# Optimization experiments

Hardware: AMD Instinct MI355X
Metric: run time of the kernel (lower is better)

Reference implementation:

```python
import jax, jax.numpy as jnp
import numpy as np
from jax import lax

EPS = 1e-08


def setup_inputs() -> dict:
    key = jax.random.key(0)
    k1, k2, k3, k4 = jax.random.split(key, 4)
    b, cin, cout, hw, kk = 32, 256, 256, 64, 3
    fan_in = cin * kk * kk
    # kaiming_normal_(a=0, mode='fan_in', nonlinearity='leaky_relu') -> gain=sqrt(2), std=sqrt(2/fan_in)
    w_std = np.sqrt(2.0 / fan_in).astype(np.float32)
    return {
        "x": jax.random.normal(k1, (b, cin, hw, hw), dtype=jnp.float32),
        "y": jax.random.normal(k2, (b, cin), dtype=jnp.float32),
        "weight": jax.random.normal(k3, (cout, cin, kk, kk), dtype=jnp.float32) * w_std,
        "bias": jax.random.normal(k4, (cout,), dtype=jnp.float32) * 0.1,
    }


def _modulated_conv(x, y, weight, bias):
    # x: [b, cin, h, w]; y: [b, cin]; weight: [cout, cin, kh, kw]; bias: [cout]
    # modulate: per-sample scale of input channels
    w = weight[None] * (y[:, None, :, None, None] + 1.0)  # [b, cout, cin, kh, kw]
    # demodulate: normalize each (sample, out-channel) filter
    d = lax.rsqrt(jnp.sum(w * w, axis=(2, 3, 4), keepdims=True) + EPS)
    w = w * d

    def conv_one(xi, wi):
        # xi: [cin, h, w]; wi: [cout, cin, kh, kw]
        out = lax.conv_general_dilated(
            xi[None], wi, window_strides=(1, 1), padding="SAME",
            dimension_numbers=("NCHW", "OIHW", "NCHW"))
        return out[0]  # [cout, h, w]

    out = jax.vmap(conv_one)(x, w)  # [b, cout, h, w]
    return out + bias[None, :, None, None]


def reference(x, y, weight, bias):
    return _modulated_conv(x, y, weight, bias)
```

## Files before the change

kernel.cpp:

```cpp
#include <hip/hip_runtime.h>
#include <hip/hip_bf16.h>

typedef __attribute__((ext_vector_type(8))) short short8;
typedef __attribute__((ext_vector_type(4))) float f32x4;

#define XT_IMG_BYTES (66*66*256*2)
#define XT_TOTAL_BYTES (32LL*XT_IMG_BYTES)
#define WM_ROW_BYTES (2304*2)
#define WM_IMG_BYTES (256*WM_ROW_BYTES)

static __device__ __forceinline__ void async16(void* lds, const void* g) {
  __builtin_amdgcn_global_load_lds((const __attribute__((address_space(1))) void*)g,
                                   (__attribute__((address_space(3))) void*)lds, 16, 0, 0);
}
static __device__ __forceinline__ ushort f2bf(float f) {
  __hip_bfloat16 h = __float2bfloat16(f);
  return *reinterpret_cast<ushort*>(&h);
}

__global__ __launch_bounds__(256) void k_prep(const float* __restrict__ x,
                                              const float* __restrict__ W,
                                              const float* __restrict__ y,
                                              ushort* __restrict__ xT,
                                              ushort* __restrict__ wmod) {
  __shared__ float smem[64][65];
  const int bid = blockIdx.x;
  const int t   = threadIdx.x;

  if (bid < 8192) {
    const int b  = bid >> 8;
    const int h  = (bid >> 2) & 63;
    const int c0 = (bid & 3) << 6;
    const int tw = t & 63, tg = t >> 6;
    const float* xp = x + (size_t)(b * 256 + c0) * 4096 + h * 64 + tw;
#pragma unroll
    for (int j = 0; j < 16; ++j) {
      int il = j * 4 + tg;
      smem[il][tw] = xp[(size_t)il * 4096];
    }
    __syncthreads();
    const int q  = t & 7;
    const int w0 = t >> 3;
    ushort* op = xT + (size_t)b * (66 * 66 * 256) + ((size_t)(h + 1) * 66 + 1) * 256 + c0;
#pragma unroll
    for (int j = 0; j < 2; ++j) {
      const int wl = j * 32 + w0;
      short8 v;
#pragma unroll
      for (int k2 = 0; k2 < 8; ++k2) v[k2] = (short)f2bf(smem[8 * q + k2][wl]);
      *(short8*)(op + (size_t)wl * 256 + 8 * q) = v;
    }
  } else if (bid < 16384) {
    float* red = &smem[0][0];
    const int bb = bid - 8192;
    const int b = bb >> 8, o = bb & 255;
    const float* wp = W + (size_t)(o * 256 + t) * 9;
    float wr[9];
#pragma unroll
    for (int r = 0; r < 9; ++r) wr[r] = wp[r];
    const float ym = y[b * 256 + t] + 1.0f;
    float ss = 0.f;
#pragma unroll
    for (int r = 0; r < 9; ++r) ss += wr[r] * wr[r];
    red[t] = ss * ym * ym;
    __syncthreads();
    for (int s = 128; s > 0; s >>= 1) {
      if (t < s) red[t] += red[t + s];
      __syncthreads();
    }
    const float sc = rsqrtf(red[0] + 1e-8f) * ym;
    ushort* op = wmod + (size_t)(b * 256 + o) * 2304 + t;
#pragma unroll
    for (int r = 0; r < 9; ++r) op[r * 256] = f2bf(wr[r] * sc);
  } else {
    const int zb = bid - 16384;
    const int b  = zb >> 3;
    const int tt = ((zb & 7) << 8) | t;
    uint4* xT4 = (uint4*)xT;
    const uint4 z = make_uint4(0u, 0u, 0u, 0u);
    uint4* base = xT4 + (size_t)b * (66 * 66 * 32);
    uint4* r0  = base;
    uint4* r65 = base + (size_t)65 * 66 * 32;
    for (int i = tt; i < 2112; i += 2048) { r0[i] = z; r65[i] = z; }
    {
      int r = (tt >> 5) + 1, c = tt & 31;
      base[((size_t)r * 66 + 0)  * 32 + c] = z;
      base[((size_t)r * 66 + 65) * 32 + c] = z;
    }
  }
}

__global__ __launch_bounds__(512, 2) void k_gemm(const ushort* __restrict__ wmod,
                                                 const ushort* __restrict__ xT,
                                                 const float* __restrict__ bias,
                                                 float* __restrict__ out) {
  __shared__ ushort ldsA[2][16384];
  __shared__ ushort ldsB[2][16384];

  const int t  = threadIdx.x;
  const int bx = blockIdx.x;
  const int xcd = bx & 7;
  const int idx = bx >> 3;
  const int b   = xcd + ((idx >> 4) << 3);
  const int tn  = idx & 15;
  const int n0  = tn << 8;
  const int h0  = tn << 2;

  const int ln = t & 15;
  const int kq = (t >> 4) & 3;
  const int wv = t >> 6;
  const int wm = wv >> 2;
  const int wn = wv & 3;

  const char* wmodB = (const char*)wmod + (size_t)b * WM_IMG_BYTES;
  const char* xTB   = (const char*)xT   + (size_t)b * XT_IMG_BYTES;

  int gAoff[4], gBoff[4];
#pragma unroll
  for (int j = 0; j < 4; ++j) {
    const int s = j * 512 + t;
    const int row = s >> 3, g = s & 7;
    gAoff[j] = row * WM_ROW_BYTES + ((g ^ (row & 7)) << 4);
    const int hr = row >> 6, wc = row & 63;
    gBoff[j] = ((h0 + hr) * 66 + wc) * 512 + ((g ^ (row & 7)) << 4);
  }

  const int swz = ln & 7;
  const int g0 = ((0 | kq) ^ swz) << 3;
  const int g1 = ((4 | kq) ^ swz) << 3;
  const int aBase = (wm * 128 + ln) * 64;
  const int bBase = (wn * 64  + ln) * 64;

  f32x4 acc[8][4];
  const f32x4 z4 = {0.f, 0.f, 0.f, 0.f};
#pragma unroll
  for (int i = 0; i < 8; ++i)
#pragma unroll
    for (int j = 0; j < 4; ++j) acc[i][j] = z4;

#define STAGE_A(KO, BUF) do {                                        \
    ushort* la_ = &ldsA[BUF][0];                                     \
    async16(la_ + (0 * 512 + t) * 8, wmodB + gAoff[0] + (KO));       \
    async16(la_ + (1 * 512 + t) * 8, wmodB + gAoff[1] + (KO));       \
    async16(la_ + (2 * 512 + t) * 8, wmodB + gAoff[2] + (KO));       \
    async16(la_ + (3 * 512 + t) * 8, wmodB + gAoff[3] + (KO));       \
  } while (0)
#define STAGE_B(KO, BUF) do {                                        \
    ushort* lb_ = &ldsB[BUF][0];                                     \
    async16(lb_ + (0 * 512 + t) * 8, xTB + gBoff[0] + (KO));         \
    async16(lb_ + (1 * 512 + t) * 8, xTB + gBoff[1] + (KO));         \
    async16(lb_ + (2 * 512 + t) * 8, xTB + gBoff[2] + (KO));         \
    async16(lb_ + (3 * 512 + t) * 8, xTB + gBoff[3] + (KO));         \
  } while (0)

#define MF(F, E, A, B) acc[F][E] = __builtin_amdgcn_mfma_f32_16x16x32_bf16(A, B, acc[F][E], 0, 0, 0)
#define FENCE() __builtin_amdgcn_sched_barrier(0)
#define BAR()   __builtin_amdgcn_s_barrier()

  STAGE_A(0, 0);
  STAGE_B(0, 0);
  asm volatile("s_waitcnt vmcnt(0)" ::: "memory");
  BAR();

  int cur = 0;
#pragma unroll 1
  for (int kt = 0; kt < 36; ++kt) {
    const int nk  = kt + 1;
    const int r_  = nk >> 2;
    const int c2_ = (nk & 3) << 7;
    const int kh_ = r_ / 3;
    const int kw_ = r_ - kh_ * 3;
    const int koA = r_ * 512 + c2_;
    const int koB = (kh_ * 66 + kw_) * 512 + c2_;
    const ushort* bufA = &ldsA[cur][0];
    const ushort* bufB = &ldsB[cur][0];
    const int nb = cur ^ 1;

    short8 A0 = *(const short8*)(bufA + aBase + 0 * 1024 + g0);
    short8 A1 = *(const short8*)(bufA + aBase + 1 * 1024 + g0);
    short8 A2 = *(const short8*)(bufA + aBase + 2 * 1024 + g0);
    short8 A3 = *(const short8*)(bufA + aBase + 3 * 1024 + g0);
    short8 B0 = *(const short8*)(bufB + bBase + 0 * 1024 + g0);
    short8 B1 = *(const short8*)(bufB + bBase + 1 * 1024 + g0);
    short8 B2 = *(const short8*)(bufB + bBase + 2 * 1024 + g0);
    short8 B3 = *(const short8*)(bufB + bBase + 3 * 1024 + g0);
    if (kt < 35) STAGE_A(koA, nb);
    FENCE(); BAR(); FENCE();
    __builtin_amdgcn_s_setprio(1);
    MF(0,0,A0,B0); MF(1,0,A1,B0); MF(2,0,A2,B0); MF(3,0,A3,B0);
    MF(0,1,A0,B1); MF(1,1,A1,B1); MF(2,1,A2,B1); MF(3,1,A3,B1);
    MF(0,2,A0,B2); MF(1,2,A1,B2); MF(2,2,A2,B2); MF(3,2,A3,B2);
    MF(0,3,A0,B3); MF(1,3,A1,B3); MF(2,3,A2,B3); MF(3,3,A3,B3);
    __builtin_amdgcn_s_setprio(0);
    FENCE(); BAR();

    short8 A4 = *(const short8*)(bufA + aBase + 4 * 1024 + g0);
    short8 A5 = *(const short8*)(bufA + aBase + 5 * 1024 + g0);
    short8 A6 = *(const short8*)(bufA + aBase + 6 * 1024 + g0);
    short8 A7 = *(const short8*)(bufA + aBase + 7 * 1024 + g0);
    if (kt < 35) STAGE_B(koB, nb);
    FENCE(); BAR(); FENCE();
    __builtin_amdgcn_s_setprio(1);
    MF(4,0,A4,B0); MF(5,0,A5,B0); MF(6,0,A6,B0); MF(7,0,A7,B0);
    MF(4,1,A4,B1); MF(5,1,A5,B1); MF(6,1,A6,B1); MF(7,1,A7,B1);
    MF(4,2,A4,B2); MF(5,2,A5,B2); MF(6,2,A6,B2); MF(7,2,A7,B2);
    MF(4,3,A4,B3); MF(5,3,A5,B3); MF(6,3,A6,B3); MF(7,3,A7,B3);
    __builtin_amdgcn_s_setprio(0);
    FENCE(); BAR();

    short8 C0 = *(const short8*)(bufA + aBase + 0 * 1024 + g1);
    short8 C1 = *(const short8*)(bufA + aBase + 1 * 1024 + g1);
    short8 C2 = *(const short8*)(bufA + aBase + 2 * 1024 + g1);
    short8 C3 = *(const short8*)(bufA + aBase + 3 * 1024 + g1);
    short8 D0 = *(const short8*)(bufB + bBase + 0 * 1024 + g1);
    short8 D1 = *(const short8*)(bufB + bBase + 1 * 1024 + g1);
    short8 D2 = *(const short8*)(bufB + bBase + 2 * 1024 + g1);
    short8 D3 = *(const short8*)(bufB + bBase + 3 * 1024 + g1);
    FENCE(); BAR(); FENCE();
    __builtin_amdgcn_s_setprio(1);
    MF(0,0,C0,D0); MF(1,0,C1,D0); MF(2,0,C2,D0); MF(3,0,C3,D0);
    MF(0,1,C0,D1); MF(1,1,C1,D1); MF(2,1,C2,D1); MF(3,1,C3,D1);
    MF(0,2,C0,D2); MF(1,2,C1,D2); MF(2,2,C2,D2); MF(3,2,C3,D2);
    MF(0,3,C0,D3); MF(1,3,C1,D3); MF(2,3,C2,D3); MF(3,3,C3,D3);
    __builtin_amdgcn_s_setprio(0);
    FENCE(); BAR();

    short8 C4 = *(const short8*)(bufA + aBase + 4 * 1024 + g1);
    short8 C5 = *(const short8*)(bufA + aBase + 5 * 1024 + g1);
    short8 C6 = *(const short8*)(bufA + aBase + 6 * 1024 + g1);
    short8 C7 = *(const short8*)(bufA + aBase + 7 * 1024 + g1);
    asm volatile("s_waitcnt vmcnt(0)" ::: "memory");
    FENCE(); BAR(); FENCE();
    __builtin_amdgcn_s_setprio(1);
    MF(4,0,C4,D0); MF(5,0,C5,D0); MF(6,0,C6,D0); MF(7,0,C7,D0);
    MF(4,1,C4,D1); MF(5,1,C5,D1); MF(6,1,C6,D1); MF(7,1,C7,D1);
    MF(4,2,C4,D2); MF(5,2,C5,D2); MF(6,2,C6,D2); MF(7,2,C7,D2);
    MF(4,3,C4,D3); MF(5,3,C5,D3); MF(6,3,C6,D3); MF(7,3,C7,D3);
    __builtin_amdgcn_s_setprio(0);
    FENCE(); BAR();

    cur = nb;
  }

  const float* bp = bias + wm * 128;
  float* outB = out + ((size_t)(b * 256 + wm * 128)) * 4096 + n0 + wn * 64 + ln;
#pragma unroll
  for (int mi = 0; mi < 8; ++mi) {
#pragma unroll
    for (int rg = 0; rg < 4; ++rg) {
      const int orow = mi * 16 + kq * 4 + rg;
      const float bv = bp[orow];
      float* po = outB + (size_t)orow * 4096;
#pragma unroll
      for (int ni = 0; ni < 4; ++ni) po[ni * 16] = acc[mi][ni][rg] + bv;
    }
  }
#undef STAGE_A
#undef STAGE_B
#undef MF
#undef FENCE
#undef BAR
}

extern "C" void kernel_launch(void* const* d_in, const int* in_sizes, int n_in,
                              void* d_out, int out_size, void* d_ws, size_t ws_size,
                              hipStream_t stream) {
  const float* x    = (const float*)d_in[0];
  const float* y    = (const float*)d_in[1];
  const float* W    = (const float*)d_in[2];
  const float* bias = (const float*)d_in[3];
  float* out = (float*)d_out;

  ushort* xT   = (ushort*)d_ws;
  ushort* wmod = (ushort*)((char*)d_ws + (size_t)XT_TOTAL_BYTES);

  k_prep<<<16640, 256, 0, stream>>>(x, W, y, xT, wmod);
  k_gemm<<<512,   512, 0, stream>>>(wmod, xT, bias, out);
}
```

Before: 374.9 us.

## Prefetch two K-tiles ahead with split loads and fewer barriers

Restructures the double-buffered main loop so that the global-to-LDS loads for the next two k-steps are issued in pieces: part of the next tile early in each iteration, the rest of the tile after next into the current buffer once its reads finish. A partial vmcnt wait is used instead of a full drain. Barriers per iteration drop from eight to two. The aim is to hide memory latency better and cut synchronisation stalls. In exchange, buffer ownership becomes much subtler, and LDS reuse races are possible if the wait counts or slot reuse are wrong.

```diff
diff --git a/kernel.cpp b/kernel.cpp
--- a/kernel.cpp
+++ b/kernel.cpp
@@ -138,43 +138,37 @@
 #pragma unroll
     for (int j = 0; j < 4; ++j) acc[i][j] = z4;
 
-#define STAGE_A(KO, BUF) do {                                        \
-    ushort* la_ = &ldsA[BUF][0];                                     \
-    async16(la_ + (0 * 512 + t) * 8, wmodB + gAoff[0] + (KO));       \
-    async16(la_ + (1 * 512 + t) * 8, wmodB + gAoff[1] + (KO));       \
-    async16(la_ + (2 * 512 + t) * 8, wmodB + gAoff[2] + (KO));       \
-    async16(la_ + (3 * 512 + t) * 8, wmodB + gAoff[3] + (KO));       \
-  } while (0)
-#define STAGE_B(KO, BUF) do {                                        \
-    ushort* lb_ = &ldsB[BUF][0];                                     \
-    async16(lb_ + (0 * 512 + t) * 8, xTB + gBoff[0] + (KO));         \
-    async16(lb_ + (1 * 512 + t) * 8, xTB + gBoff[1] + (KO));         \
-    async16(lb_ + (2 * 512 + t) * 8, xTB + gBoff[2] + (KO));         \
-    async16(lb_ + (3 * 512 + t) * 8, xTB + gBoff[3] + (KO));         \
-  } while (0)
+#define LOAD_A(J, KO, BUF) async16(&ldsA[BUF][0] + ((J) * 512 + t) * 8, wmodB + gAoff[J] + (KO))
+#define LOAD_B(J, KO, BUF) async16(&ldsB[BUF][0] + ((J) * 512 + t) * 8, xTB   + gBoff[J] + (KO))
 
 #define MF(F, E, A, B) acc[F][E] = __builtin_amdgcn_mfma_f32_16x16x32_bf16(A, B, acc[F][E], 0, 0, 0)
 #define FENCE() __builtin_amdgcn_sched_barrier(0)
 #define BAR()   __builtin_amdgcn_s_barrier()
 
-  STAGE_A(0, 0);
-  STAGE_B(0, 0);
-  asm volatile("s_waitcnt vmcnt(0)" ::: "memory");
-  BAR();
-
-  int cur = 0;
+  LOAD_A(0, 0, 0); LOAD_A(1, 0, 0); LOAD_A(2, 0, 0); LOAD_A(3, 0, 0);
+  LOAD_B(0, 0, 0); LOAD_B(1, 0, 0); LOAD_B(2, 0, 0); LOAD_B(3, 0, 0);
+  {
+    const int koA1 = 0 * 512 + 128;
+    const int koB1 = (0 * 66 + 0) * 512 + 128;
+    LOAD_A(0, koA1, 1); LOAD_A(2, koA1, 1);
+    LOAD_B(0, koB1, 1); LOAD_B(1, koB1, 1); LOAD_B(2, koB1, 1); LOAD_B(3, koB1, 1);
+  }
+  asm volatile("s_waitcnt vmcnt(6)" ::: "memory");
+  FENCE(); BAR(); FENCE();
+
 #pragma unroll 1
   for (int kt = 0; kt < 36; ++kt) {
-    const int nk  = kt + 1;
-    const int r_  = nk >> 2;
-    const int c2_ = (nk & 3) << 7;
-    const int kh_ = r_ / 3;
-    const int kw_ = r_ - kh_ * 3;
-    const int koA = r_ * 512 + c2_;
-    const int koB = (kh_ * 66 + kw_) * 512 + c2_;
+    const int cur = kt & 1, nb = cur ^ 1;
     const ushort* bufA = &ldsA[cur][0];
     const ushort* bufB = &ldsB[cur][0];
-    const int nb = cur ^ 1;
+
+    const int n1 = kt + 1;
+    const int koA1 = (n1 >> 2) * 512 + ((n1 & 3) << 7);
+    const int n2 = kt + 2;
+    const int r2 = n2 >> 2;
+    const int kh2 = r2 / 3, kw2 = r2 - kh2 * 3;
+    const int koA2 = r2 * 512 + ((n2 & 3) << 7);
+    const int koB2 = (kh2 * 66 + kw2) * 512 + ((n2 & 3) << 7);
 
     short8 A0 = *(const short8*)(bufA + aBase + 0 * 1024 + g0);
     short8 A1 = *(const short8*)(bufA + aBase + 1 * 1024 + g0);
@@ -184,29 +178,25 @@
     short8 B1 = *(const short8*)(bufB + bBase + 1 * 1024 + g0);
     short8 B2 = *(const short8*)(bufB + bBase + 2 * 1024 + g0);
     short8 B3 = *(const short8*)(bufB + bBase + 3 * 1024 + g0);
-    if (kt < 35) STAGE_A(koA, nb);
-    FENCE(); BAR(); FENCE();
+    if (kt < 35) { LOAD_A(1, koA1, nb); LOAD_A(3, koA1, nb); }
     __builtin_amdgcn_s_setprio(1);
     MF(0,0,A0,B0); MF(1,0,A1,B0); MF(2,0,A2,B0); MF(3,0,A3,B0);
     MF(0,1,A0,B1); MF(1,1,A1,B1); MF(2,1,A2,B1); MF(3,1,A3,B1);
     MF(0,2,A0,B2); MF(1,2,A1,B2); MF(2,2,A2,B2); MF(3,2,A3,B2);
     MF(0,3,A0,B3); MF(1,3,A1,B3); MF(2,3,A2,B3); MF(3,3,A3,B3);
     __builtin_amdgcn_s_setprio(0);
-    FENCE(); BAR();
 
     short8 A4 = *(const short8*)(bufA + aBase + 4 * 1024 + g0);
     short8 A5 = *(const short8*)(bufA + aBase + 5 * 1024 + g0);
     short8 A6 = *(const short8*)(bufA + aBase + 6 * 1024 + g0);
     short8 A7 = *(const short8*)(bufA + aBase + 7 * 1024 + g0);
-    if (kt < 35) STAGE_B(koB, nb);
-    FENCE(); BAR(); FENCE();
     __builtin_amdgcn_s_setprio(1);
     MF(4,0,A4,B0); MF(5,0,A5,B0); MF(6,0,A6,B0); MF(7,0,A7,B0);
     MF(4,1,A4,B1); MF(5,1,A5,B1); MF(6,1,A6,B1); MF(7,1,A7,B1);
     MF(4,2,A4,B2); MF(5,2,A5,B2); MF(6,2,A6,B2); MF(7,2,A7,B2);
     MF(4,3,A4,B3); MF(5,3,A5,B3); MF(6,3,A6,B3); MF(7,3,A7,B3);
     __builtin_amdgcn_s_setprio(0);
-    FENCE(); BAR();
+    FENCE();
 
     short8 C0 = *(const short8*)(bufA + aBase + 0 * 1024 + g1);
     short8 C1 = *(const short8*)(bufA + aBase + 1 * 1024 + g1);
@@ -216,30 +206,37 @@
     short8 D1 = *(const short8*)(bufB + bBase + 1 * 1024 + g1);
     short8 D2 = *(const short8*)(bufB + bBase + 2 * 1024 + g1);
     short8 D3 = *(const short8*)(bufB + bBase + 3 * 1024 + g1);
-    FENCE(); BAR(); FENCE();
     __builtin_amdgcn_s_setprio(1);
     MF(0,0,C0,D0); MF(1,0,C1,D0); MF(2,0,C2,D0); MF(3,0,C3,D0);
     MF(0,1,C0,D1); MF(1,1,C1,D1); MF(2,1,C2,D1); MF(3,1,C3,D1);
     MF(0,2,C0,D2); MF(1,2,C1,D2); MF(2,2,C2,D2); MF(3,2,C3,D2);
     MF(0,3,C0,D3); MF(1,3,C1,D3); MF(2,3,C2,D3); MF(3,3,C3,D3);
     __builtin_amdgcn_s_setprio(0);
-    FENCE(); BAR();
+
+    FENCE(); BAR(); FENCE();
 
     short8 C4 = *(const short8*)(bufA + aBase + 4 * 1024 + g1);
     short8 C5 = *(const short8*)(bufA + aBase + 5 * 1024 + g1);
     short8 C6 = *(const short8*)(bufA + aBase + 6 * 1024 + g1);
     short8 C7 = *(const short8*)(bufA + aBase + 7 * 1024 + g1);
-    asm volatile("s_waitcnt vmcnt(0)" ::: "memory");
-    FENCE(); BAR(); FENCE();
+    if (kt < 34) {
+      LOAD_A(0, koA2, cur); LOAD_A(2, koA2, cur);
+      LOAD_B(0, koB2, cur); LOAD_B(1, koB2, cur);
+      LOAD_B(2, koB2, cur); LOAD_B(3, koB2, cur);
+    }
     __builtin_amdgcn_s_setprio(1);
     MF(4,0,C4,D0); MF(5,0,C5,D0); MF(6,0,C6,D0); MF(7,0,C7,D0);
     MF(4,1,C4,D1); MF(5,1,C5,D1); MF(6,1,C6,D1); MF(7,1,C7,D1);
     MF(4,2,C4,D2); MF(5,2,C5,D2); MF(6,2,C6,D2); MF(7,2,C7,D2);
     MF(4,3,C4,D3); MF(5,3,C5,D3); MF(6,3,C6,D3); MF(7,3,C7,D3);
     __builtin_amdgcn_s_setprio(0);
-    FENCE(); BAR();
-
-    cur = nb;
+
+    if (kt < 34) {
+      asm volatile("s_waitcnt vmcnt(6)" ::: "memory");
+    } else {
+      asm volatile("s_waitcnt vmcnt(0)" ::: "memory");
+    }
+    FENCE(); BAR(); FENCE();
   }
 
   const float* bp = bias + wm * 128;
@@ -255,8 +252,8 @@
       for (int ni = 0; ni < 4; ++ni) po[ni * 16] = acc[mi][ni][rg] + bv;
     }
   }
-#undef STAGE_A
-#undef STAGE_B
+#undef LOAD_A
+#undef LOAD_B
 #undef MF
 #undef FENCE
 #undef BAR
```

Result: no change. 373.8 us (-0.3%).
